# Optimization experiments

Hardware: AMD Instinct MI355X
Metric: run time of the kernel (lower is better)

Reference implementation:

```python
import jax, jax.numpy as jnp
import numpy as np
from jax import lax

FIRE_RATE = 0.5       # forward() default fire_rate
INPUT_CHANNELS = 1    # module input_channels
EPS = 1e-5            # BatchNorm eps


def p4_conv_z2(x, w, b):
    """Z2 -> P4 group conv. x: [B,I,H,W], w: [O,I,k,k] -> [B,O,4,H,W]."""
    # rotate the spatial kernel by r*90deg for each of the 4 output orientations
    ws = jnp.stack([jnp.rot90(w, r, axes=(2, 3)) for r in range(4)], axis=1)  # [O,4,I,k,k]
    O, _, I, k, _ = ws.shape
    y = lax.conv_general_dilated(x, ws.reshape(O * 4, I, k, k), (1, 1), 'SAME',
                                 dimension_numbers=('NCHW', 'OIHW', 'NCHW'))
    B, _, H, W = x.shape
    return y.reshape(B, O, 4, H, W) + b[None, :, None, None, None]


def p4_conv_p4(x, w, b):
    """P4 -> P4 group conv. x: [B,I,4,H,W], w: [O,I,4,k,k] -> [B,O,4,H,W]."""
    # for output orientation r: cyclic-shift input-orientation axis by r and rotate spatially by r
    ws = jnp.stack([jnp.rot90(jnp.roll(w, r, axis=2), r, axes=(3, 4)) for r in range(4)],
                   axis=1)  # [O,4,I,4,k,k]
    O, _, I, _, k, _ = ws.shape
    B, _, _, H, W = x.shape
    y = lax.conv_general_dilated(x.reshape(B, I * 4, H, W),
                                 ws.reshape(O * 4, I * 4, k, k), (1, 1), 'SAME',
                                 dimension_numbers=('NCHW', 'OIHW', 'NCHW'))
    return y.reshape(B, O, 4, H, W) + b[None, :, None, None, None]


def _update(x_nhwc, w1, b1, gamma, beta, w2, b2, key):
    x = jnp.transpose(x_nhwc, (0, 3, 1, 2))            # [B,C,H,W]
    y = p4_conv_z2(x, w1, b1)                          # [B,Ch,4,H,W]
    # BatchNorm3d (batch stats, affine): normalize each channel over (B, rot, H, W)
    mu = jnp.mean(y, axis=(0, 2, 3, 4), keepdims=True)
    var = jnp.var(y, axis=(0, 2, 3, 4), keepdims=True)
    y = gamma[None, :, None, None, None] * (y - mu) * lax.rsqrt(var + EPS) \
        + beta[None, :, None, None, None]
    y = jax.nn.relu(y)
    dy = p4_conv_p4(y, w2, b2).mean(axis=2)            # mean over rotation axis -> [B,C,H,W]
    B, _, H, W = dy.shape
    mask = (jax.random.uniform(key, (B, 1, H, W), dtype=dy.dtype) > FIRE_RATE).astype(dy.dtype)
    x = x + dy * mask
    return jnp.transpose(x, (0, 2, 3, 1))              # back to [B,H,W,C]


def nca_forward(x, w1, b1, gamma, beta, w2, b2, steps):
    base_key = jax.random.key(42)
    for step in range(steps):
        x2 = _update(x, w1, b1, gamma, beta, w2, b2, jax.random.fold_in(base_key, step))
        # first input_channels are clamped to the original input
        x = jnp.concatenate((x[..., :INPUT_CHANNELS], x2[..., INPUT_CHANNELS:]), axis=-1)
    return x


def setup_inputs() -> dict:
    key = jax.random.key(0)
    ks = jax.random.split(key, 6)
    B, H, W = 8, 192, 192
    C = 16            # channel_n
    CH = 128 // 8     # base_hidden_size = hidden_size // 8
    K = 7             # kernel_size
    # fan-in scaled init (matches nn.Conv2d-style scaling)
    x = jax.random.normal(ks[0], (B, H, W, C), dtype=jnp.float32)
    w1 = jax.random.normal(ks[1], (CH, C, K, K), dtype=jnp.float32) / np.sqrt(C * K * K)
    b1 = jnp.zeros((CH,), dtype=jnp.float32)
    gamma = jnp.ones((CH,), dtype=jnp.float32)
    beta = jnp.zeros((CH,), dtype=jnp.float32)
    w2 = jax.random.normal(ks[2], (C, CH, 4, 1, 1), dtype=jnp.float32) / np.sqrt(CH * 4)
    b2 = jnp.zeros((C,), dtype=jnp.float32)
    return {"x": x, "w1": w1, "b1": b1, "gamma": gamma, "beta": beta,
            "w2": w2, "b2": b2, "steps": 10}


def reference(x, w1, b1, gamma, beta, w2, b2, steps):
    return nca_forward(x, w1, b1, gamma, beta, w2, b2, steps)
```

## Files before the change

kernel.cpp:

```cpp
#include <hip/hip_runtime.h>
#include <stdint.h>

#define HH 192
#define WW 192
#define BB 8
#define NSTEP 10
#define HWSZ (HH*WW)
#define NPIX (BB*HWSZ)
#define TILE_W 24
#define TILE_H 16
#define XROWS 22
#define XCOLS 30
#define RSU   488
#define XBUFU (XROWS*RSU)
#define NKS   25
#define NBLK  (8*12*8)

typedef _Float16 f16x8 __attribute__((ext_vector_type(8)));
typedef float    f32x4 __attribute__((ext_vector_type(4)));

union PackU { ushort u[8]; uint4 v; };

__host__ __device__ inline void tf2x32(uint32_t k0, uint32_t k1,
                                       uint32_t x0, uint32_t x1,
                                       uint32_t &o0, uint32_t &o1) {
  const uint32_t k2 = k0 ^ k1 ^ 0x1BD11BDAu;
  x0 += k0; x1 += k1;
#define TFR(r) { x0 += x1; x1 = (x1 << (r)) | (x1 >> (32 - (r))); x1 ^= x0; }
  TFR(13) TFR(15) TFR(26) TFR(6)
  x0 += k1; x1 += k2 + 1u;
  TFR(17) TFR(29) TFR(16) TFR(24)
  x0 += k2; x1 += k0 + 2u;
  TFR(13) TFR(15) TFR(26) TFR(6)
  x0 += k0; x1 += k1 + 3u;
  TFR(17) TFR(29) TFR(16) TFR(24)
  x0 += k1; x1 += k2 + 4u;
  TFR(13) TFR(15) TFR(26) TFR(6)
  x0 += k2; x1 += k0 + 5u;
#undef TFR
  o0 = x0; o1 = x1;
}

__device__ inline void split2048(float v, ushort &h, ushort &l) {
  _Float16 hi = (_Float16)v;
  float r = (v - (float)hi) * 2048.0f;
  _Float16 lo = (_Float16)r;
  h = __builtin_bit_cast(ushort, hi);
  l = __builtin_bit_cast(ushort, lo);
}

__global__ void k_prep_wfrag(const float* __restrict__ w1,
                             ushort* __restrict__ wfh, ushort* __restrict__ wfl) {
  int idx = blockIdx.x * 256 + threadIdx.x;
  if (idx >= NKS * 4 * 64) return;
  const int lane = idx & 63;
  const int sm = idx >> 6;
  const int s = sm >> 2, mt = sm & 3;
  const int m = lane & 15, g = lane >> 4;
  const int j = mt * 16 + m, co = j >> 2, r = j & 3;
  const int t = 2 * s + (g >> 1);
  PackU ph, pl;
#pragma unroll
  for (int e = 0; e < 8; ++e) {
    const int ci = 8 * (g & 1) + e;
    float wv = 0.f;
    if (t < 49) {
      const int ky = t / 7, kx = t - (t / 7) * 7;
      int a = ky, b = kx;
      for (int i = 0; i < r; ++i) { int na = b, nb = 6 - a; a = na; b = nb; }
      wv = w1[((co * 16 + ci) * 7 + a) * 7 + b];
    }
    split2048(wv, ph.u[e], pl.u[e]);
  }
  ((uint4*)wfh)[sm * 64 + lane] = ph.v;
  ((uint4*)wfl)[sm * 64 + lane] = pl.v;
}

__global__ void k_prep_w2(const float* __restrict__ w2, float* __restrict__ wsum) {
  int idx = threadIdx.x;
  float s = 0.f;
  for (int t = 0; t < 4; ++t) s += w2[idx * 4 + t];
  wsum[idx] = 0.25f * s;
}

__global__ __launch_bounds__(256, 1) void k_conv1(
    const float* __restrict__ xsrc,
    const ushort* __restrict__ wfh,
    const ushort* __restrict__ wfl,
    const float* __restrict__ b1,
    float* __restrict__ y,
    float* __restrict__ partials)
{
  __shared__ __align__(16) ushort xsm[2 * XBUFU];
  __shared__ float red2[4][32];
  const int tid = threadIdx.x;
  const int lane = tid & 63, wid = tid >> 6;
  const int x0 = blockIdx.x * TILE_W, y0 = blockIdx.y * TILE_H;
  const int b = blockIdx.z;
  const int bid = (b * gridDim.y + blockIdx.y) * gridDim.x + blockIdx.x;

  for (int p = tid; p < XROWS * XCOLS * 2; p += 256) {
    const int half = p & 1, t2 = p >> 1;
    const int lr = t2 / XCOLS, lc = t2 - (t2 / XCOLS) * XCOLS;
    const int gy = y0 + lr - 3, gx = x0 + lc - 3;
    float4 v0, v1;
    if ((unsigned)gy < (unsigned)HH && (unsigned)gx < (unsigned)WW) {
      const float4* px = (const float4*)(xsrc + ((size_t)b * HWSZ + (size_t)gy * WW + gx) * 16 + half * 8);
      v0 = px[0]; v1 = px[1];
    } else {
      v0 = v1 = make_float4(0.f, 0.f, 0.f, 0.f);
    }
    const float xv[8] = {v0.x, v0.y, v0.z, v0.w, v1.x, v1.y, v1.z, v1.w};
    PackU h, l;
#pragma unroll
    for (int c = 0; c < 8; ++c) split2048(xv[c], h.u[c], l.u[c]);
    const int ub = lr * RSU + lc * 16 + half * 8;
    *(uint4*)&xsm[ub] = h.v;
    *(uint4*)&xsm[XBUFU + ub] = l.v;
  }
  __syncthreads();

  const int n = lane & 15;
  const int q = lane >> 4;
  const int h = q & 1;
  int bU[6];
#pragma unroll
  for (int st = 0; st < 6; ++st) bU[st] = n * RSU + (6 * wid + st) * 16 + h * 8;

  const f16x8* __restrict__ WAh = (const f16x8*)wfh;
  const f16x8* __restrict__ WAl = (const f16x8*)wfl;

  float bias[4];
#pragma unroll
  for (int mt = 0; mt < 4; ++mt) bias[mt] = b1[mt * 4 + q];

  f32x4 accH[6][4], accC[6][4];
#pragma unroll
  for (int st = 0; st < 6; ++st)
#pragma unroll
    for (int mt = 0; mt < 4; ++mt) {
      const float bv = bias[mt];
      accH[st][mt] = (f32x4){bv, bv, bv, bv};
      accC[st][mt] = (f32x4){0.f, 0.f, 0.f, 0.f};
    }

  f16x8 Ah[2][4], Al[2][4];
  f16x8 Bh[2][6], Bl[2][6];

  auto boff = [&](int sp) -> int {
    const int t0 = 2 * sp, t1 = t0 + 1;
    const int o0 = (t0 / 7) * RSU + (t0 % 7) * 16;
    const int o1 = (t1 < 49) ? (t1 / 7) * RSU + (t1 % 7) * 16 : 0;
    return (lane < 32) ? o0 : o1;
  };

#pragma unroll
  for (int mt = 0; mt < 4; ++mt) {
    Ah[0][mt] = WAh[mt * 64 + lane];
    Al[0][mt] = WAl[mt * 64 + lane];
  }
  {
    const int off = boff(0);
#pragma unroll
    for (int st = 0; st < 6; ++st) {
      Bh[0][st] = *(const f16x8*)&xsm[bU[st] + off];
      Bl[0][st] = *(const f16x8*)&xsm[XBUFU + bU[st] + off];
    }
  }

#pragma unroll
  for (int s = 0; s < NKS; ++s) {
    const int cb = s & 1, nb = cb ^ 1;
    if (s < NKS - 1) {
#pragma unroll
      for (int mt = 0; mt < 4; ++mt) {
        const int f = ((s + 1) * 4 + mt) * 64 + lane;
        Ah[nb][mt] = WAh[f];
        Al[nb][mt] = WAl[f];
      }
      const int off = boff(s + 1);
#pragma unroll
      for (int st = 0; st < 6; ++st) {
        Bh[nb][st] = *(const f16x8*)&xsm[bU[st] + off];
        Bl[nb][st] = *(const f16x8*)&xsm[XBUFU + bU[st] + off];
      }
    }
    __builtin_amdgcn_sched_barrier(0);
#pragma unroll
    for (int mt = 0; mt < 4; ++mt) {
#pragma unroll
      for (int st = 0; st < 6; ++st)
        accH[st][mt] = __builtin_amdgcn_mfma_f32_16x16x32_f16(Ah[cb][mt], Bh[cb][st], accH[st][mt], 0, 0, 0);
    }
#pragma unroll
    for (int mt = 0; mt < 4; ++mt) {
#pragma unroll
      for (int st = 0; st < 6; ++st)
        accC[st][mt] = __builtin_amdgcn_mfma_f32_16x16x32_f16(Ah[cb][mt], Bl[cb][st], accC[st][mt], 0, 0, 0);
    }
#pragma unroll
    for (int mt = 0; mt < 4; ++mt) {
#pragma unroll
      for (int st = 0; st < 6; ++st)
        accC[st][mt] = __builtin_amdgcn_mfma_f32_16x16x32_f16(Al[cb][mt], Bh[cb][st], accC[st][mt], 0, 0, 0);
    }
  }

  float sC[4] = {0.f, 0.f, 0.f, 0.f}, qC[4] = {0.f, 0.f, 0.f, 0.f};
#pragma unroll
  for (int st = 0; st < 6; ++st) {
    const size_t pix = (size_t)b * HWSZ + (size_t)(y0 + n) * WW + (x0 + 6 * wid + st);
#pragma unroll
    for (int mt = 0; mt < 4; ++mt) {
      f32x4 res = accH[st][mt] + accC[st][mt] * 4.8828125e-4f;
      *(float4*)(y + pix * 64 + mt * 16 + q * 4) =
          make_float4(res[0], res[1], res[2], res[3]);
#pragma unroll
      for (int r = 0; r < 4; ++r) { sC[mt] += res[r]; qC[mt] += res[r] * res[r]; }
    }
  }
#pragma unroll
  for (int mt = 0; mt < 4; ++mt) {
    float s = sC[mt], s2 = qC[mt];
#pragma unroll
    for (int off = 1; off <= 8; off <<= 1) {
      s += __shfl_xor(s, off); s2 += __shfl_xor(s2, off);
    }
    if (n == 0) {
      red2[wid][(mt * 4 + q) * 2] = s;
      red2[wid][(mt * 4 + q) * 2 + 1] = s2;
    }
  }
  __syncthreads();
  if (tid < 32) {
    float v = red2[0][tid] + red2[1][tid] + red2[2][tid] + red2[3][tid];
    partials[(size_t)bid * 32 + tid] = v;
  }
}

__global__ __launch_bounds__(256) void k_bnstats(
    const float* __restrict__ partials,
    const float* __restrict__ gamma, const float* __restrict__ beta,
    float* __restrict__ stats)
{
  const int c = blockIdx.x;
  const int tid = threadIdx.x;
  float s = 0.f, s2 = 0.f;
  for (int i = tid; i < NBLK; i += 256) {
    s  += partials[(size_t)i * 32 + 2 * c];
    s2 += partials[(size_t)i * 32 + 2 * c + 1];
  }
  __shared__ float rs[256], rs2[256];
  rs[tid] = s; rs2[tid] = s2;
  __syncthreads();
  for (int off = 128; off > 0; off >>= 1) {
    if (tid < off) { rs[tid] += rs[tid + off]; rs2[tid] += rs2[tid + off]; }
    __syncthreads();
  }
  if (tid == 0) {
    const float N = (float)BB * 4.f * HH * WW;
    const float mu = rs[0] / N;
    const float var = rs2[0] / N - mu * mu;
    const float rstd = rsqrtf(var + 1e-5f);
    const float sc = gamma[c] * rstd;
    stats[2 * c]     = sc;
    stats[2 * c + 1] = beta[c] - mu * sc;
  }
}

__global__ __launch_bounds__(256) void k_update(
    const float* __restrict__ xsrc,
    const float* __restrict__ y,
    const float* __restrict__ stats,
    const float* __restrict__ wsum,
    const float* __restrict__ b2,
    float* __restrict__ xdst,
    uint32_t fk0, uint32_t fk1)
{
  __shared__ float sss[32];
  __shared__ float sws[256];
  __shared__ float sb2[16];
  const int tid = threadIdx.x;
  sws[tid] = wsum[tid];
  if (tid < 32) sss[tid] = stats[tid];
  if (tid < 16) sb2[tid] = b2[tid];
  __syncthreads();

  const size_t pix = (size_t)blockIdx.x * 256 + tid;
  const float4* yp = (const float4*)(y + pix * 64);
  float ysum[16];
#pragma unroll
  for (int c = 0; c < 16; ++c) {
    const float4 v = yp[c];
    const float sc = sss[2 * c], sh = sss[2 * c + 1];
    ysum[c] = fmaxf(fmaf(sc, v.x, sh), 0.f) + fmaxf(fmaf(sc, v.y, sh), 0.f)
            + fmaxf(fmaf(sc, v.z, sh), 0.f) + fmaxf(fmaf(sc, v.w, sh), 0.f);
  }

  uint32_t h0, h1;
  tf2x32(fk0, fk1, 0u, (uint32_t)pix, h0, h1);
  const uint32_t bits = h0 ^ h1;
  const float u = __uint_as_float((bits >> 9) | 0x3f800000u) - 1.0f;
  const float m = (u > 0.5f) ? 1.0f : 0.0f;

  const float4* xp = (const float4*)(xsrc + pix * 16);
  float4* op = (float4*)(xdst + pix * 16);
#pragma unroll
  for (int qq = 0; qq < 4; ++qq) {
    const float4 xv = xp[qq];
    float d[4];
#pragma unroll
    for (int jj = 0; jj < 4; ++jj) {
      const int o = 4 * qq + jj;
      float s = sb2[o];
#pragma unroll
      for (int c = 0; c < 16; ++c) s = fmaf(sws[o * 16 + c], ysum[c], s);
      d[jj] = s;
    }
    float4 r;
    r.x = xv.x + d[0] * m;
    r.y = xv.y + d[1] * m;
    r.z = xv.z + d[2] * m;
    r.w = xv.w + d[3] * m;
    if (qq == 0) r.x = xv.x;
    op[qq] = r;
  }
}

extern "C" void kernel_launch(void* const* d_in, const int* in_sizes, int n_in,
                              void* d_out, int out_size, void* d_ws, size_t ws_size,
                              hipStream_t stream) {
  const float* x_in  = (const float*)d_in[0];
  const float* w1    = (const float*)d_in[1];
  const float* b1    = (const float*)d_in[2];
  const float* gamma = (const float*)d_in[3];
  const float* beta  = (const float*)d_in[4];
  const float* w2    = (const float*)d_in[5];
  const float* b2    = (const float*)d_in[6];
  float* out = (float*)d_out;

  float* ws       = (float*)d_ws;
  float* y        = ws;
  ushort* wfh     = (ushort*)(y + (size_t)NPIX * 64);
  ushort* wfl     = wfh + NKS * 2048;
  float* wsum     = (float*)(wfl + NKS * 2048);
  float* partials = wsum + 256;
  float* stats    = partials + NBLK * 32;

  k_prep_wfrag<<<NKS, 256, 0, stream>>>(w1, wfh, wfl);
  k_prep_w2<<<1, 256, 0, stream>>>(w2, wsum);

  for (int s = 0; s < NSTEP; ++s) {
    const float* xsrc = (s == 0) ? x_in : out;
    k_conv1<<<dim3(WW / TILE_W, HH / TILE_H, BB), 256, 0, stream>>>(xsrc, wfh, wfl, b1, y, partials);
    k_bnstats<<<16, 256, 0, stream>>>(partials, gamma, beta, stats);
    uint32_t fk0, fk1;
    tf2x32(0u, 42u, 0u, (uint32_t)s, fk0, fk1);
    k_update<<<NPIX / 256, 256, 0, stream>>>(xsrc, y, stats, wsum, b2, out, fk0, fk1);
  }
}
```

Measured before the change: 1.077 ms.

## Switch conv1 to 32x32x16 MFMA with 16x16 tiles and per-tap K

Rewrites the first group convolution's inner loop to use 32x32x16 f16 MFMA instructions. Each tap now covers the 16 input channels as K, which removes the padded 50th tap the earlier two-taps-per-step scheme needed. The tile shrinks to 16x16 pixels and the launch bound allows two blocks per CU, so the grid grows and occupancy can rise. Weight fragments and output/stat layouts are rebuilt for the new accumulator format, and s_setprio is added around the MFMA bursts. In exchange, smaller tiles mean more halo loading and conversion per output pixel.

```diff
diff --git a/kernel.cpp b/kernel.cpp
--- a/kernel.cpp
+++ b/kernel.cpp
@@ -7,17 +7,16 @@
 #define NSTEP 10
 #define HWSZ (HH*WW)
 #define NPIX (BB*HWSZ)
-#define TILE_W 24
-#define TILE_H 16
+#define TILE 16
 #define XROWS 22
-#define XCOLS 30
-#define RSU   488
+#define XCOLS 22
+#define RSU   360
 #define XBUFU (XROWS*RSU)
-#define NKS   25
-#define NBLK  (8*12*8)
+#define NTAP  49
+#define NBLK  (12*12*8)
 
 typedef _Float16 f16x8 __attribute__((ext_vector_type(8)));
-typedef float    f32x4 __attribute__((ext_vector_type(4)));
+typedef float    f32x16 __attribute__((ext_vector_type(16)));
 
 union PackU { ushort u[8]; uint4 v; };
 
@@ -52,28 +51,24 @@
 __global__ void k_prep_wfrag(const float* __restrict__ w1,
                              ushort* __restrict__ wfh, ushort* __restrict__ wfl) {
   int idx = blockIdx.x * 256 + threadIdx.x;
-  if (idx >= NKS * 4 * 64) return;
+  if (idx >= NTAP * 2 * 64) return;
   const int lane = idx & 63;
-  const int sm = idx >> 6;
-  const int s = sm >> 2, mt = sm & 3;
-  const int m = lane & 15, g = lane >> 4;
-  const int j = mt * 16 + m, co = j >> 2, r = j & 3;
-  const int t = 2 * s + (g >> 1);
+  const int ft = idx >> 6;
+  const int t = ft >> 1, tile = ft & 1;
+  const int m = lane & 31;
+  const int j = tile * 32 + m, co = j >> 2, r = j & 3;
+  const int cibase = (lane >> 5) * 8;
+  const int ky = t / 7, kx = t - (t / 7) * 7;
+  int a = ky, b = kx;
+  for (int i = 0; i < r; ++i) { int na = b, nb = 6 - a; a = na; b = nb; }
   PackU ph, pl;
 #pragma unroll
   for (int e = 0; e < 8; ++e) {
-    const int ci = 8 * (g & 1) + e;
-    float wv = 0.f;
-    if (t < 49) {
-      const int ky = t / 7, kx = t - (t / 7) * 7;
-      int a = ky, b = kx;
-      for (int i = 0; i < r; ++i) { int na = b, nb = 6 - a; a = na; b = nb; }
-      wv = w1[((co * 16 + ci) * 7 + a) * 7 + b];
-    }
-    split2048(wv, ph.u[e], pl.u[e]);
-  }
-  ((uint4*)wfh)[sm * 64 + lane] = ph.v;
-  ((uint4*)wfl)[sm * 64 + lane] = pl.v;
+    const int ci = cibase + e;
+    split2048(w1[((co * 16 + ci) * 7 + a) * 7 + b], ph.u[e], pl.u[e]);
+  }
+  ((uint4*)wfh)[ft * 64 + lane] = ph.v;
+  ((uint4*)wfl)[ft * 64 + lane] = pl.v;
 }
 
 __global__ void k_prep_w2(const float* __restrict__ w2, float* __restrict__ wsum) {
@@ -83,7 +78,7 @@
   wsum[idx] = 0.25f * s;
 }
 
-__global__ __launch_bounds__(256, 1) void k_conv1(
+__global__ __launch_bounds__(256, 2) void k_conv1(
     const float* __restrict__ xsrc,
     const ushort* __restrict__ wfh,
     const ushort* __restrict__ wfl,
@@ -95,7 +90,7 @@
   __shared__ float red2[4][32];
   const int tid = threadIdx.x;
   const int lane = tid & 63, wid = tid >> 6;
-  const int x0 = blockIdx.x * TILE_W, y0 = blockIdx.y * TILE_H;
+  const int x0 = blockIdx.x * TILE, y0 = blockIdx.y * TILE;
   const int b = blockIdx.z;
   const int bid = (b * gridDim.y + blockIdx.y) * gridDim.x + blockIdx.x;
 
@@ -120,117 +115,131 @@
   }
   __syncthreads();
 
-  const int n = lane & 15;
-  const int q = lane >> 4;
-  const int h = q & 1;
-  int bU[6];
-#pragma unroll
-  for (int st = 0; st < 6; ++st) bU[st] = n * RSU + (6 * wid + st) * 16 + h * 8;
+  const int n5 = lane & 31;
+  const int row = lane & 15;
+  const int colof = (lane >> 4) & 1;
+  const int hi5 = lane >> 5;
+  int bU[2];
+#pragma unroll
+  for (int g = 0; g < 2; ++g)
+    bU[g] = row * RSU + (wid * 4 + 2 * g + colof) * 16 + hi5 * 8;
 
   const f16x8* __restrict__ WAh = (const f16x8*)wfh;
   const f16x8* __restrict__ WAl = (const f16x8*)wfl;
 
-  float bias[4];
-#pragma unroll
-  for (int mt = 0; mt < 4; ++mt) bias[mt] = b1[mt * 4 + q];
-
-  f32x4 accH[6][4], accC[6][4];
-#pragma unroll
-  for (int st = 0; st < 6; ++st)
-#pragma unroll
-    for (int mt = 0; mt < 4; ++mt) {
-      const float bv = bias[mt];
-      accH[st][mt] = (f32x4){bv, bv, bv, bv};
-      accC[st][mt] = (f32x4){0.f, 0.f, 0.f, 0.f};
-    }
-
-  f16x8 Ah[2][4], Al[2][4];
-  f16x8 Bh[2][6], Bl[2][6];
-
-  auto boff = [&](int sp) -> int {
-    const int t0 = 2 * sp, t1 = t0 + 1;
-    const int o0 = (t0 / 7) * RSU + (t0 % 7) * 16;
-    const int o1 = (t1 < 49) ? (t1 / 7) * RSU + (t1 % 7) * 16 : 0;
-    return (lane < 32) ? o0 : o1;
-  };
-
-#pragma unroll
-  for (int mt = 0; mt < 4; ++mt) {
-    Ah[0][mt] = WAh[mt * 64 + lane];
-    Al[0][mt] = WAl[mt * 64 + lane];
-  }
-  {
-    const int off = boff(0);
-#pragma unroll
-    for (int st = 0; st < 6; ++st) {
-      Bh[0][st] = *(const f16x8*)&xsm[bU[st] + off];
-      Bl[0][st] = *(const f16x8*)&xsm[XBUFU + bU[st] + off];
-    }
-  }
-
-#pragma unroll
-  for (int s = 0; s < NKS; ++s) {
-    const int cb = s & 1, nb = cb ^ 1;
-    if (s < NKS - 1) {
-#pragma unroll
-      for (int mt = 0; mt < 4; ++mt) {
-        const int f = ((s + 1) * 4 + mt) * 64 + lane;
-        Ah[nb][mt] = WAh[f];
-        Al[nb][mt] = WAl[f];
-      }
-      const int off = boff(s + 1);
-#pragma unroll
-      for (int st = 0; st < 6; ++st) {
-        Bh[nb][st] = *(const f16x8*)&xsm[bU[st] + off];
-        Bl[nb][st] = *(const f16x8*)&xsm[XBUFU + bU[st] + off];
+  float bias[2][4];
+#pragma unroll
+  for (int tile = 0; tile < 2; ++tile)
+#pragma unroll
+    for (int q2 = 0; q2 < 4; ++q2) bias[tile][q2] = b1[tile * 8 + hi5 + 2 * q2];
+
+  f32x16 accH[2][2], accC[2][2];
+#pragma unroll
+  for (int g = 0; g < 2; ++g)
+#pragma unroll
+    for (int tile = 0; tile < 2; ++tile) {
+#pragma unroll
+      for (int reg = 0; reg < 16; ++reg) {
+        accH[g][tile][reg] = bias[tile][reg >> 2];
+        accC[g][tile][reg] = 0.f;
+      }
+    }
+
+  f16x8 Ah[2][2], Al[2][2];
+  f16x8 Bh[2][2], Bl[2][2];
+
+  auto boff = [&](int t) -> int { return (t / 7) * RSU + (t % 7) * 16; };
+
+#pragma unroll
+  for (int tile = 0; tile < 2; ++tile) {
+    Ah[0][tile] = WAh[tile * 64 + lane];
+    Al[0][tile] = WAl[tile * 64 + lane];
+  }
+#pragma unroll
+  for (int g = 0; g < 2; ++g) {
+    Bh[0][g] = *(const f16x8*)&xsm[bU[g]];
+    Bl[0][g] = *(const f16x8*)&xsm[XBUFU + bU[g]];
+  }
+
+#pragma unroll
+  for (int t = 0; t < NTAP; ++t) {
+    const int cb = t & 1, nb = cb ^ 1;
+    if (t < NTAP - 1) {
+#pragma unroll
+      for (int tile = 0; tile < 2; ++tile) {
+        const int f = ((t + 1) * 2 + tile) * 64 + lane;
+        Ah[nb][tile] = WAh[f];
+        Al[nb][tile] = WAl[f];
+      }
+      const int off = boff(t + 1);
+#pragma unroll
+      for (int g = 0; g < 2; ++g) {
+        Bh[nb][g] = *(const f16x8*)&xsm[bU[g] + off];
+        Bl[nb][g] = *(const f16x8*)&xsm[XBUFU + bU[g] + off];
       }
     }
     __builtin_amdgcn_sched_barrier(0);
-#pragma unroll
-    for (int mt = 0; mt < 4; ++mt) {
-#pragma unroll
-      for (int st = 0; st < 6; ++st)
-        accH[st][mt] = __builtin_amdgcn_mfma_f32_16x16x32_f16(Ah[cb][mt], Bh[cb][st], accH[st][mt], 0, 0, 0);
-    }
-#pragma unroll
-    for (int mt = 0; mt < 4; ++mt) {
-#pragma unroll
-      for (int st = 0; st < 6; ++st)
-        accC[st][mt] = __builtin_amdgcn_mfma_f32_16x16x32_f16(Ah[cb][mt], Bl[cb][st], accC[st][mt], 0, 0, 0);
-    }
-#pragma unroll
-    for (int mt = 0; mt < 4; ++mt) {
-#pragma unroll
-      for (int st = 0; st < 6; ++st)
-        accC[st][mt] = __builtin_amdgcn_mfma_f32_16x16x32_f16(Al[cb][mt], Bh[cb][st], accC[st][mt], 0, 0, 0);
-    }
-  }
-
-  float sC[4] = {0.f, 0.f, 0.f, 0.f}, qC[4] = {0.f, 0.f, 0.f, 0.f};
-#pragma unroll
-  for (int st = 0; st < 6; ++st) {
-    const size_t pix = (size_t)b * HWSZ + (size_t)(y0 + n) * WW + (x0 + 6 * wid + st);
-#pragma unroll
-    for (int mt = 0; mt < 4; ++mt) {
-      f32x4 res = accH[st][mt] + accC[st][mt] * 4.8828125e-4f;
-      *(float4*)(y + pix * 64 + mt * 16 + q * 4) =
-          make_float4(res[0], res[1], res[2], res[3]);
-#pragma unroll
-      for (int r = 0; r < 4; ++r) { sC[mt] += res[r]; qC[mt] += res[r] * res[r]; }
-    }
-  }
-#pragma unroll
-  for (int mt = 0; mt < 4; ++mt) {
-    float s = sC[mt], s2 = qC[mt];
-#pragma unroll
-    for (int off = 1; off <= 8; off <<= 1) {
-      s += __shfl_xor(s, off); s2 += __shfl_xor(s2, off);
-    }
-    if (n == 0) {
-      red2[wid][(mt * 4 + q) * 2] = s;
-      red2[wid][(mt * 4 + q) * 2 + 1] = s2;
-    }
-  }
+    __builtin_amdgcn_s_setprio(1);
+#pragma unroll
+    for (int g = 0; g < 2; ++g)
+#pragma unroll
+      for (int tile = 0; tile < 2; ++tile)
+        accH[g][tile] = __builtin_amdgcn_mfma_f32_32x32x16_f16(Ah[cb][tile], Bh[cb][g], accH[g][tile], 0, 0, 0);
+#pragma unroll
+    for (int g = 0; g < 2; ++g)
+#pragma unroll
+      for (int tile = 0; tile < 2; ++tile)
+        accC[g][tile] = __builtin_amdgcn_mfma_f32_32x32x16_f16(Ah[cb][tile], Bl[cb][g], accC[g][tile], 0, 0, 0);
+#pragma unroll
+    for (int g = 0; g < 2; ++g)
+#pragma unroll
+      for (int tile = 0; tile < 2; ++tile)
+        accC[g][tile] = __builtin_amdgcn_mfma_f32_32x32x16_f16(Al[cb][tile], Bh[cb][g], accC[g][tile], 0, 0, 0);
+    __builtin_amdgcn_s_setprio(0);
+  }
+
+  float sC[2][4], qC[2][4];
+#pragma unroll
+  for (int tile = 0; tile < 2; ++tile)
+#pragma unroll
+    for (int q2 = 0; q2 < 4; ++q2) { sC[tile][q2] = 0.f; qC[tile][q2] = 0.f; }
+
+#pragma unroll
+  for (int g = 0; g < 2; ++g) {
+    const size_t pix = (size_t)b * HWSZ + (size_t)(y0 + row) * WW + (x0 + wid * 4 + 2 * g + colof);
+#pragma unroll
+    for (int tile = 0; tile < 2; ++tile) {
+      f32x16 res;
+#pragma unroll
+      for (int reg = 0; reg < 16; ++reg)
+        res[reg] = accH[g][tile][reg] + accC[g][tile][reg] * 4.8828125e-4f;
+#pragma unroll
+      for (int q2 = 0; q2 < 4; ++q2) {
+        *(float4*)(y + pix * 64 + tile * 32 + 8 * q2 + 4 * hi5) =
+            make_float4(res[4 * q2], res[4 * q2 + 1], res[4 * q2 + 2], res[4 * q2 + 3]);
+#pragma unroll
+        for (int i = 0; i < 4; ++i) {
+          const float v = res[4 * q2 + i];
+          sC[tile][q2] += v; qC[tile][q2] += v * v;
+        }
+      }
+    }
+  }
+#pragma unroll
+  for (int tile = 0; tile < 2; ++tile)
+#pragma unroll
+    for (int q2 = 0; q2 < 4; ++q2) {
+      float s = sC[tile][q2], q = qC[tile][q2];
+#pragma unroll
+      for (int off = 1; off <= 16; off <<= 1) {
+        s += __shfl_xor(s, off); q += __shfl_xor(q, off);
+      }
+      if (n5 == 0) {
+        const int c = tile * 8 + 2 * q2 + hi5;
+        red2[wid][2 * c] = s;
+        red2[wid][2 * c + 1] = q;
+      }
+    }
   __syncthreads();
   if (tid < 32) {
     float v = red2[0][tid] + red2[1][tid] + red2[2][tid] + red2[3][tid];
@@ -342,17 +351,17 @@
   float* ws       = (float*)d_ws;
   float* y        = ws;
   ushort* wfh     = (ushort*)(y + (size_t)NPIX * 64);
-  ushort* wfl     = wfh + NKS * 2048;
-  float* wsum     = (float*)(wfl + NKS * 2048);
+  ushort* wfl     = wfh + NTAP * 2 * 64 * 8;
+  float* wsum     = (float*)(wfl + NTAP * 2 * 64 * 8);
   float* partials = wsum + 256;
   float* stats    = partials + NBLK * 32;
 
-  k_prep_wfrag<<<NKS, 256, 0, stream>>>(w1, wfh, wfl);
+  k_prep_wfrag<<<25, 256, 0, stream>>>(w1, wfh, wfl);
   k_prep_w2<<<1, 256, 0, stream>>>(w2, wsum);
 
   for (int s = 0; s < NSTEP; ++s) {
     const float* xsrc = (s == 0) ? x_in : out;
-    k_conv1<<<dim3(WW / TILE_W, HH / TILE_H, BB), 256, 0, stream>>>(xsrc, wfh, wfl, b1, y, partials);
+    k_conv1<<<dim3(WW / TILE, HH / TILE, BB), 256, 0, stream>>>(xsrc, wfh, wfl, b1, y, partials);
     k_bnstats<<<16, 256, 0, stream>>>(partials, gamma, beta, stats);
     uint32_t fk0, fk1;
     tf2x32(0u, 42u, 0u, (uint32_t)s, fk0, fk1);
```

Result: slower. 1.243 ms (+15.4%).
